# Performance work log

Measured on AMD Instinct MI355X. Metric: run time of the kernel, lower is better.

The kernel has to match this reference:

```python
import jax, jax.numpy as jnp
import numpy as np

N = 100000        # nodes
E = 1600000       # directed edges (before self loops)
F = 128           # input node features
H1, H2, H3 = 64, 32, 16
G = 64            # graphs in batch
EPS = 1e-5
NEG_SLOPE = 0.2


def setup_inputs():
    key = jax.random.key(0)
    ks = jax.random.split(key, 16)
    def rn(k, shape, scale=1.0):
        return jax.random.normal(k, shape, dtype=jnp.float32) * scale
    inp = {}
    inp['x'] = rn(ks[0], (N, F))
    inp['edge_index'] = jax.random.randint(ks[1], (2, E), 0, N)
    inp['batch'] = jnp.sort(jax.random.randint(ks[2], (N,), 0, G))
    dims = [(F, H1), (H1, H2), (H2, H3)]
    i = 3
    for li, (fi, fo) in enumerate(dims, start=1):
        s = 1.0 / np.sqrt(fi)
        kk = jax.random.split(ks[i], 3)
        inp[f'Wl{li}'] = rn(kk[0], (fi, fo), s)
        inp[f'bl{li}'] = jnp.zeros((fo,), jnp.float32)
        inp[f'Wr{li}'] = rn(kk[1], (fi, fo), s)
        inp[f'br{li}'] = jnp.zeros((fo,), jnp.float32)
        inp[f'att{li}'] = rn(kk[2], (fo,), 1.0 / np.sqrt(fo))
        inp[f'bias{li}'] = jnp.zeros((fo,), jnp.float32)
        inp[f'gamma{li}'] = jnp.ones((fo,), jnp.float32)
        inp[f'beta{li}'] = jnp.zeros((fo,), jnp.float32)
        i += 1
    inp['linW'] = rn(ks[i], (H3, 1), 0.25)
    inp['linb'] = jnp.zeros((1,), jnp.float32)
    return inp


def _gatv2(x, Wl, bl, Wr, br, att, bias, src, dst):
    # PyG GATv2Conv, heads=1: e_ij = a^T LeakyReLU(Wl x_j + Wr x_i)
    xl = x @ Wl + bl                         # [N, H] source transform
    xr = x @ Wr + br                         # [N, H] target transform
    e = jax.nn.leaky_relu(xl[src] + xr[dst], NEG_SLOPE) @ att   # [E']
    # numerically stable segment softmax over incoming edges of dst
    emax = jax.ops.segment_max(e, dst, num_segments=N)
    w = jnp.exp(e - emax[dst])
    denom = jax.ops.segment_sum(w, dst, num_segments=N)
    alpha = w / (denom[dst] + 1e-16)         # [E']
    out = jax.ops.segment_sum(alpha[:, None] * xl[src], dst, num_segments=N)
    return out + bias


def _batchnorm(x, gamma, beta):
    mu = jnp.mean(x, axis=0)
    var = jnp.var(x, axis=0)
    return (x - mu) * jax.lax.rsqrt(var + EPS) * gamma + beta


def reference(x, edge_index, batch,
              Wl1, bl1, Wr1, br1, att1, bias1, gamma1, beta1,
              Wl2, bl2, Wr2, br2, att2, bias2, gamma2, beta2,
              Wl3, bl3, Wr3, br3, att3, bias3, gamma3, beta3,
              linW, linb):
    # add self loops once (PyG GATv2Conv default add_self_loops=True)
    loops = jnp.arange(N, dtype=edge_index.dtype)
    src = jnp.concatenate([edge_index[0], loops])
    dst = jnp.concatenate([edge_index[1], loops])

    h = _gatv2(x, Wl1, bl1, Wr1, br1, att1, bias1, src, dst)
    h = jax.nn.relu(_batchnorm(h, gamma1, beta1))
    h = _gatv2(h, Wl2, bl2, Wr2, br2, att2, bias2, src, dst)
    h = jax.nn.relu(_batchnorm(h, gamma2, beta2))
    h = _gatv2(h, Wl3, bl3, Wr3, br3, att3, bias3, src, dst)
    h = jax.nn.relu(_batchnorm(h, gamma3, beta3))

    # global mean pool over graphs
    sums = jax.ops.segment_sum(h, batch, num_segments=G)          # [G, 16]
    cnts = jax.ops.segment_sum(jnp.ones((N,), h.dtype), batch, num_segments=G)
    pooled = sums / jnp.maximum(cnts, 1.0)[:, None]
    return pooled @ linW + linb                                   # [G, 1]
```

## Files before the change

### kernel.cpp

```cpp
#include <hip/hip_runtime.h>
#include <hip/hip_bf16.h>


static constexpr int G_ = 64;

__device__ __forceinline__ float bf2f(unsigned short u) {
  union { unsigned int i; float f; } c;
  c.i = ((unsigned int)u) << 16;
  return c.f;
}
__device__ __forceinline__ unsigned short f2bf(float f) {
  union { float f; unsigned int i; } c;
  c.f = f;
  unsigned int r = c.i + 0x7FFFu + ((c.i >> 16) & 1u);
  return (unsigned short)(r >> 16);
}

__global__ __launch_bounds__(256) void pack_all(
    const float* __restrict__ Wl1, const float* __restrict__ Wr1,
    const float* __restrict__ bl1, const float* __restrict__ br1,
    const float* __restrict__ Wl2, const float* __restrict__ Wr2,
    const float* __restrict__ bl2, const float* __restrict__ br2,
    const float* __restrict__ Wl3, const float* __restrict__ Wr3,
    const float* __restrict__ bl3, const float* __restrict__ br3,
    float* __restrict__ Wc1, float* __restrict__ bc1,
    float* __restrict__ Wc2, float* __restrict__ bc2,
    float* __restrict__ Wc3, float* __restrict__ bc3) {
  int i = blockIdx.x * 256 + threadIdx.x;
  if (i < 128 * 128) { int k = i >> 7, c = i & 127;
    Wc1[i] = (c < 64) ? Wl1[k * 64 + c] : Wr1[k * 64 + c - 64]; }
  if (i < 128) bc1[i] = (i < 64) ? bl1[i] : br1[i - 64];
  if (i < 64 * 64) { int k = i >> 6, c = i & 63;
    Wc2[i] = (c < 32) ? Wl2[k * 32 + c] : Wr2[k * 32 + c - 32]; }
  if (i < 64) bc2[i] = (i < 32) ? bl2[i] : br2[i - 32];
  if (i < 32 * 32) { int k = i >> 5, c = i & 31;
    Wc3[i] = (c < 16) ? Wl3[k * 16 + c] : Wr3[k * 16 + c - 16]; }
  if (i < 32) bc3[i] = (i < 16) ? bl3[i] : br3[i - 16];
}

template <int FI>
__global__ __launch_bounds__(256) void transpose_nf(
    const float* __restrict__ A, float* __restrict__ At, int N) {
  __shared__ float s[64][65];
  int n0 = blockIdx.x * 64, k0 = blockIdx.y * 64;
  int tid = threadIdx.x;
  for (int idx = tid; idx < 64 * 16; idx += 256) {
    int n = idx >> 4, c = idx & 15;
    float4 v = make_float4(0.f, 0.f, 0.f, 0.f);
    if (n0 + n < N)
      v = *reinterpret_cast<const float4*>(&A[(size_t)(n0 + n) * FI + k0 + c * 4]);
    s[n][c * 4 + 0] = v.x; s[n][c * 4 + 1] = v.y;
    s[n][c * 4 + 2] = v.z; s[n][c * 4 + 3] = v.w;
  }
  __syncthreads();
  for (int idx = tid; idx < 64 * 16; idx += 256) {
    int k = idx >> 4, c = idx & 15;
    int n = c * 4;
    if (n0 + n + 3 < N) {
      float4 v = make_float4(s[n][k], s[n + 1][k], s[n + 2][k], s[n + 3][k]);
      *reinterpret_cast<float4*>(&At[(size_t)(k0 + k) * N + n0 + n]) = v;
    } else {
      for (int j = 0; j < 4; j++)
        if (n0 + n + j < N) At[(size_t)(k0 + k) * N + n0 + n + j] = s[n + j][k];
    }
  }
}

__global__ __launch_bounds__(256) void edge_hist(
    const int* __restrict__ ei, int* __restrict__ deg, int E, int Etot, int N) {
  int p = blockIdx.x & 7;
  int q = blockIdx.x >> 3;
  int nbq = gridDim.x >> 3;
  float scale = 8.0f / (float)N;
  for (int i = q * 256 + threadIdx.x; i < Etot; i += nbq * 256) {
    int dst = (i < E) ? ei[E + i] : (i - E);
    int pp = min((int)((float)dst * scale), 7);
    if (pp == p) atomicAdd(&deg[dst], 1);
  }
}

__global__ __launch_bounds__(256) void scan1(
    const int* __restrict__ deg, int* __restrict__ part, int* __restrict__ bsums, int n) {
  __shared__ int ts[256];
  int t = threadIdx.x, b = blockIdx.x;
  int base = b * 1024 + t * 4;
  int d[4];
#pragma unroll
  for (int q = 0; q < 4; q++) d[q] = (base + q < n) ? deg[base + q] : 0;
  int s = d[0] + d[1] + d[2] + d[3];
  ts[t] = s;
  __syncthreads();
  for (int o = 1; o < 256; o <<= 1) {
    int v = (t >= o) ? ts[t - o] : 0;
    __syncthreads();
    ts[t] += v;
    __syncthreads();
  }
  int incl = ts[t];
  if (t == 255) bsums[b] = incl;
  int run = incl - s;
#pragma unroll
  for (int q = 0; q < 4; q++) {
    if (base + q < n) part[base + q] = run;
    run += d[q];
  }
}

__global__ void scan2(int* bsums, int nb) {
  __shared__ int s[256];
  int t = threadIdx.x;
  int v = (t < nb) ? bsums[t] : 0;
  s[t] = v;
  __syncthreads();
  for (int o = 1; o < 256; o <<= 1) {
    int u = (t >= o) ? s[t - o] : 0;
    __syncthreads();
    s[t] += u;
    __syncthreads();
  }
  if (t < nb) bsums[t] = s[t] - v;
}

__global__ __launch_bounds__(256) void scan3(
    int* __restrict__ rp, int* __restrict__ cur, const int* __restrict__ bsums,
    int n, int Etot) {
  int i = blockIdx.x * 256 + threadIdx.x;
  if (i < n) {
    int v = rp[i] + bsums[i >> 10];
    rp[i] = v; cur[i] = v;
  }
  if (i == 0) rp[n] = Etot;
}

__global__ __launch_bounds__(256) void scatter_edges(
    const int* __restrict__ ei, int* __restrict__ cur, int* __restrict__ ssrc,
    int E, int Etot, int N) {
  int p = blockIdx.x & 7;
  int q = blockIdx.x >> 3;
  int nbq = gridDim.x >> 3;
  float scale = 8.0f / (float)N;
  for (int i = q * 256 + threadIdx.x; i < Etot; i += nbq * 256) {
    int dst = (i < E) ? ei[E + i] : (i - E);
    int pp = min((int)((float)dst * scale), 7);
    if (pp != p) continue;
    int src = (i < E) ? ei[i] : (i - E);
    int pos = atomicAdd(&cur[dst], 1);
    ssrc[pos] = src;
  }
}

template <int FI, int FO>
__global__ __launch_bounds__(256) void gemm_fmaj2(
    const float* __restrict__ At, const float* __restrict__ Wcat,
    const float* __restrict__ bcat, unsigned short* __restrict__ Cb, int N) {
  constexpr int KC = 32;
  constexpr int CT = FO / 16;
  __shared__ float As[KC * 128];
  __shared__ float Ws[KC * FO];
  int tid = threadIdx.x;
  int ng = tid & 15;
  int hg = tid >> 4;
  int n0 = blockIdx.x * 128;
  bool full = (n0 + 128 <= N);

  float acc[8][CT];
#pragma unroll
  for (int i = 0; i < 8; i++)
#pragma unroll
    for (int j = 0; j < CT; j++) acc[i][j] = 0.f;

  for (int kc = 0; kc < FI; kc += KC) {
    __syncthreads();
    {
      int r = tid >> 5;
      int c = (tid & 31) * 4;
      for (int rr = r; rr < KC; rr += 8) {
        float4 v;
        if (full) {
          v = *reinterpret_cast<const float4*>(&At[(size_t)(kc + rr) * N + n0 + c]);
        } else {
          float tmp[4];
#pragma unroll
          for (int j = 0; j < 4; j++)
            tmp[j] = (n0 + c + j < N) ? At[(size_t)(kc + rr) * N + n0 + c + j] : 0.f;
          v = make_float4(tmp[0], tmp[1], tmp[2], tmp[3]);
        }
        *reinterpret_cast<float4*>(&As[rr * 128 + c]) = v;
      }
    }
    for (int idx = tid; idx < KC * FO / 4; idx += 256)
      *reinterpret_cast<float4*>(&Ws[idx * 4]) =
          *reinterpret_cast<const float4*>(&Wcat[kc * FO + idx * 4]);
    __syncthreads();
#pragma unroll
    for (int kk = 0; kk < KC; kk++) {
      float4 alo = *reinterpret_cast<float4*>(&As[kk * 128 + 4 * ng]);
      float4 ahi = *reinterpret_cast<float4*>(&As[kk * 128 + 64 + 4 * ng]);
      float a[8] = {alo.x, alo.y, alo.z, alo.w, ahi.x, ahi.y, ahi.z, ahi.w};
      float w[CT];
#pragma unroll
      for (int j = 0; j < CT; j++) w[j] = Ws[kk * FO + hg * CT + j];
#pragma unroll
      for (int i = 0; i < 8; i++)
#pragma unroll
        for (int j = 0; j < CT; j++) acc[i][j] = fmaf(a[i], w[j], acc[i][j]);
    }
  }

  float b[CT];
#pragma unroll
  for (int j = 0; j < CT; j++) b[j] = bcat[hg * CT + j];
#pragma unroll
  for (int i = 0; i < 8; i++) {
    int n = n0 + ((i < 4) ? (4 * ng + i) : (64 + 4 * ng + (i - 4)));
    if (n < N) {
      unsigned int u[CT / 2];
#pragma unroll
      for (int j2 = 0; j2 < CT / 2; j2++) {
        unsigned int lo = f2bf(acc[i][2 * j2] + b[2 * j2]);
        unsigned int hi = f2bf(acc[i][2 * j2 + 1] + b[2 * j2 + 1]);
        u[j2] = lo | (hi << 16);
      }
      unsigned short* dst = &Cb[(size_t)n * FO + hg * CT];
      if constexpr (CT == 8) {
        *reinterpret_cast<uint4*>(dst) = make_uint4(u[0], u[1], u[2], u[3]);
      } else if constexpr (CT == 4) {
        *reinterpret_cast<uint2*>(dst) = make_uint2(u[0], u[1]);
      } else {
        *reinterpret_cast<unsigned int*>(dst) = u[0];
      }
    }
  }
}

__device__ __forceinline__ float lrelu02(float z) {
  return (z > 0.f) ? z : 0.2f * z;
}

template <int H, bool UN2>
__global__ __launch_bounds__(256) void gat_agg2(
    const unsigned short* __restrict__ xlr, const float* __restrict__ att,
    const float* __restrict__ bias, const int* __restrict__ rp,
    const int* __restrict__ ssrc, float* __restrict__ out, int N) {
  constexpr int L = H / 4;
  constexpr int C = 64 / L;
  int v = blockIdx.x * 4 + (threadIdx.x >> 6);
  if (v >= N) return;
  int lane = threadIdx.x & 63;
  int fl = lane % L;
  int sub = lane / L;

  ushort4 qr = *reinterpret_cast<const ushort4*>(&xlr[(size_t)v * (2 * H) + H + fl * 4]);
  float xr0 = bf2f(qr.x), xr1 = bf2f(qr.y), xr2 = bf2f(qr.z), xr3 = bf2f(qr.w);
  const float4 a4 = *reinterpret_cast<const float4*>(&att[fl * 4]);
  int beg = rp[v], end = rp[v + 1];

  float mA = -3.0e38f, dA = 0.f;
  float4 accA = make_float4(0.f, 0.f, 0.f, 0.f);
  float mB = -3.0e38f, dB = 0.f;
  float4 accB = make_float4(0.f, 0.f, 0.f, 0.f);

  constexpr int STEP = UN2 ? 2 * C : C;

  for (int j = beg + sub; j < end; j += STEP) {
    {
      int u = ssrc[j];
      ushort4 q = *reinterpret_cast<const ushort4*>(&xlr[(size_t)u * (2 * H) + fl * 4]);
      float x0 = bf2f(q.x), x1 = bf2f(q.y), x2 = bf2f(q.z), x3 = bf2f(q.w);
      float t = a4.x * lrelu02(x0 + xr0);
      t = fmaf(a4.y, lrelu02(x1 + xr1), t);
      t = fmaf(a4.z, lrelu02(x2 + xr2), t);
      t = fmaf(a4.w, lrelu02(x3 + xr3), t);
#pragma unroll
      for (int o = L / 2; o >= 1; o >>= 1) t += __shfl_xor(t, o);
      float diff = t - mA;
      if (diff > 8.f) {
        float sc = __expf(-diff);
        dA *= sc;
        accA.x *= sc; accA.y *= sc; accA.z *= sc; accA.w *= sc;
        mA = t; diff = 0.f;
      }
      float w = __expf(diff);
      dA += w;
      accA.x = fmaf(w, x0, accA.x);
      accA.y = fmaf(w, x1, accA.y);
      accA.z = fmaf(w, x2, accA.z);
      accA.w = fmaf(w, x3, accA.w);
    }
    if (UN2) {
      int j2 = j + C;
      if (j2 < end) {
        int u = ssrc[j2];
        ushort4 q = *reinterpret_cast<const ushort4*>(&xlr[(size_t)u * (2 * H) + fl * 4]);
        float x0 = bf2f(q.x), x1 = bf2f(q.y), x2 = bf2f(q.z), x3 = bf2f(q.w);
        float t = a4.x * lrelu02(x0 + xr0);
        t = fmaf(a4.y, lrelu02(x1 + xr1), t);
        t = fmaf(a4.z, lrelu02(x2 + xr2), t);
        t = fmaf(a4.w, lrelu02(x3 + xr3), t);
#pragma unroll
        for (int o = L / 2; o >= 1; o >>= 1) t += __shfl_xor(t, o);
        float diff = t - mB;
        if (diff > 8.f) {
          float sc = __expf(-diff);
          dB *= sc;
          accB.x *= sc; accB.y *= sc; accB.z *= sc; accB.w *= sc;
          mB = t; diff = 0.f;
        }
        float w = __expf(diff);
        dB += w;
        accB.x = fmaf(w, x0, accB.x);
        accB.y = fmaf(w, x1, accB.y);
        accB.z = fmaf(w, x2, accB.z);
        accB.w = fmaf(w, x3, accB.w);
      }
    }
  }

  if (UN2) {
    float mn = fmaxf(mA, mB);
    float s1 = __expf(mA - mn), s2 = __expf(mB - mn);
    dA = dA * s1 + dB * s2;
    accA.x = accA.x * s1 + accB.x * s2;
    accA.y = accA.y * s1 + accB.y * s2;
    accA.z = accA.z * s1 + accB.z * s2;
    accA.w = accA.w * s1 + accB.w * s2;
    mA = mn;
  }

#pragma unroll
  for (int o = L; o < 64; o <<= 1) {
    float mo = __shfl_xor(mA, o);
    float d2 = __shfl_xor(dA, o);
    float ax = __shfl_xor(accA.x, o);
    float ay = __shfl_xor(accA.y, o);
    float az = __shfl_xor(accA.z, o);
    float aw = __shfl_xor(accA.w, o);
    float mn = fmaxf(mA, mo);
    float s1 = __expf(mA - mn), s2 = __expf(mo - mn);
    dA = dA * s1 + d2 * s2;
    accA.x = accA.x * s1 + ax * s2;
    accA.y = accA.y * s1 + ay * s2;
    accA.z = accA.z * s1 + az * s2;
    accA.w = accA.w * s1 + aw * s2;
    mA = mn;
  }

  if (lane < L) {
    float inv = 1.f / (dA + 1e-16f);
    const float4 b4 = *reinterpret_cast<const float4*>(&bias[fl * 4]);
    float4 o4 = make_float4(fmaf(accA.x, inv, b4.x), fmaf(accA.y, inv, b4.y),
                            fmaf(accA.z, inv, b4.z), fmaf(accA.w, inv, b4.w));
    *reinterpret_cast<float4*>(&out[(size_t)v * H + fl * 4]) = o4;
  }
}

template <int H>
__global__ __launch_bounds__(256) void bn_stats(
    const float* __restrict__ X, float* __restrict__ stats, int N) {
  __shared__ float ls[256], ls2[256];
  int tid = threadIdx.x;
  int h = tid % H;
  constexpr int RPB = 256 / H;
  int r0 = blockIdx.x * RPB + tid / H;
  float s = 0.f, s2 = 0.f;
  for (int n = r0; n < N; n += gridDim.x * RPB) {
    float val = X[(size_t)n * H + h];
    s += val; s2 += val * val;
  }
  ls[tid] = s; ls2[tid] = s2;
  __syncthreads();
  if (tid < H) {
    for (int g = 1; g < RPB; g++) { s += ls[tid + g * H]; s2 += ls2[tid + g * H]; }
    atomicAdd(&stats[h], s);
    atomicAdd(&stats[H + h], s2);
  }
}

__global__ void bn_finalize(
    const float* __restrict__ stats, const float* __restrict__ gamma,
    const float* __restrict__ beta, float* __restrict__ ss, int H, int N) {
  int h = threadIdx.x;
  if (h < H) {
    float mean = stats[h] / (float)N;
    float var = stats[H + h] / (float)N - mean * mean;
    float istd = rsqrtf(var + 1e-5f);
    float sc = gamma[h] * istd;
    ss[h] = sc;
    ss[H + h] = beta[h] - mean * sc;
  }
}

template <int H>
__global__ __launch_bounds__(256) void bn_apply_T(
    const float* __restrict__ X, const float* __restrict__ ss,
    float* __restrict__ Yt, int N) {
  __shared__ float s[64][65];
  int n0 = blockIdx.x * 64;
  int tid = threadIdx.x;
  for (int idx = tid; idx < 64 * (H / 4); idx += 256) {
    int n = idx / (H / 4), c = idx % (H / 4);
    float4 v = make_float4(0.f, 0.f, 0.f, 0.f);
    if (n0 + n < N)
      v = *reinterpret_cast<const float4*>(&X[(size_t)(n0 + n) * H + c * 4]);
    s[n][c * 4 + 0] = v.x; s[n][c * 4 + 1] = v.y;
    s[n][c * 4 + 2] = v.z; s[n][c * 4 + 3] = v.w;
  }
  __syncthreads();
  for (int idx = tid; idx < H * 16; idx += 256) {
    int k = idx >> 4, c = idx & 15;
    int n = c * 4;
    float sc = ss[k], sh = ss[H + k];
    float t0 = s[n + 0][k] * sc + sh;
    float t1 = s[n + 1][k] * sc + sh;
    float t2 = s[n + 2][k] * sc + sh;
    float t3 = s[n + 3][k] * sc + sh;
    float4 v = make_float4(t0 > 0.f ? t0 : 0.f, t1 > 0.f ? t1 : 0.f,
                           t2 > 0.f ? t2 : 0.f, t3 > 0.f ? t3 : 0.f);
    if (n0 + n + 3 < N) {
      *reinterpret_cast<float4*>(&Yt[(size_t)k * N + n0 + n]) = v;
    } else {
      float tv[4] = {v.x, v.y, v.z, v.w};
      for (int j = 0; j < 4; j++)
        if (n0 + n + j < N) Yt[(size_t)k * N + n0 + n + j] = tv[j];
    }
  }
}

__global__ __launch_bounds__(256) void pool_kernel(
    const float* __restrict__ X, const float* __restrict__ ss,
    const int* __restrict__ batch, float* __restrict__ pool,
    float* __restrict__ cnt, int N) {
  __shared__ float lp[G_ * 16];
  __shared__ float lc[G_];
  int tid = threadIdx.x;
  for (int j = tid; j < G_ * 16; j += 256) lp[j] = 0.f;
  if (tid < G_) lc[tid] = 0.f;
  __syncthreads();
  int tot = N * 16;
  for (int i = blockIdx.x * 256 + tid; i < tot; i += gridDim.x * 256) {
    int n = i >> 4, h = i & 15;
    int g = batch[n];
    float t = X[i] * ss[h] + ss[16 + h];
    t = (t > 0.f) ? t : 0.f;
    atomicAdd(&lp[g * 16 + h], t);
    if (h == 0) atomicAdd(&lc[g], 1.0f);
  }
  __syncthreads();
  for (int j = tid; j < G_ * 16; j += 256) atomicAdd(&pool[j], lp[j]);
  if (tid < G_) atomicAdd(&cnt[tid], lc[tid]);
}

__global__ void final_linear(
    const float* __restrict__ pool, const float* __restrict__ cnt,
    const float* __restrict__ linW, const float* __restrict__ linb,
    float* __restrict__ out) {
  int g = threadIdx.x;
  if (g < G_) {
    float c = fmaxf(cnt[g], 1.0f);
    float acc = 0.f;
    for (int h = 0; h < 16; h++) acc += (pool[g * 16 + h] / c) * linW[h];
    out[g] = acc + linb[0];
  }
}

extern "C" void kernel_launch(void* const* d_in, const int* in_sizes, int n_in,
                              void* d_out, int out_size, void* d_ws, size_t ws_size,
                              hipStream_t stream) {
  const float* x = (const float*)d_in[0];
  const int* ei = (const int*)d_in[1];
  const int* batch = (const int*)d_in[2];
  const int N = in_sizes[0] / 128;
  const int E = in_sizes[1] / 2;
  const int Etot = E + N;

  char* wsb = (char*)d_ws;
  size_t off = 0;
  auto alloc = [&](size_t bytes) -> void* {
    void* p = wsb + off;
    off += (bytes + 255) & ~(size_t)255;
    return p;
  };
  float* R0 = (float*)alloc((size_t)128 * N * 4);
  unsigned short* R1b = (unsigned short*)alloc((size_t)128 * N * 2);
  float* R2 = (float*)alloc((size_t)64 * N * 4);
  int* row_ptr = (int*)alloc((size_t)(N + 1) * 4);
  int* cursor = (int*)alloc((size_t)N * 4);
  int* bsums = (int*)alloc(4096);
  int* ssrc = (int*)alloc((size_t)Etot * 4);
  float* Wc1 = (float*)alloc(16384 * 4);  float* bc1 = (float*)alloc(128 * 4);
  float* Wc2 = (float*)alloc(4096 * 4);   float* bc2 = (float*)alloc(64 * 4);
  float* Wc3 = (float*)alloc(1024 * 4);   float* bc3 = (float*)alloc(32 * 4);
  float* ss = (float*)alloc(128 * 4);
  size_t zelems = (size_t)N + 3 * 128 + G_ * 16 + G_;
  char* zb = (char*)alloc(zelems * 4);
  int* deg = (int*)zb;
  float* stats1 = (float*)(zb + (size_t)N * 4);
  float* stats2 = stats1 + 128;
  float* stats3 = stats2 + 128;
  float* pool = stats3 + 128;
  float* cnt = pool + G_ * 16;

  const float* Wl1 = (const float*)d_in[3];  const float* bl1 = (const float*)d_in[4];
  const float* Wr1 = (const float*)d_in[5];  const float* br1 = (const float*)d_in[6];
  const float* att1 = (const float*)d_in[7]; const float* bias1 = (const float*)d_in[8];
  const float* g1 = (const float*)d_in[9];   const float* b1 = (const float*)d_in[10];
  const float* Wl2 = (const float*)d_in[11]; const float* bl2 = (const float*)d_in[12];
  const float* Wr2 = (const float*)d_in[13]; const float* br2 = (const float*)d_in[14];
  const float* att2 = (const float*)d_in[15]; const float* bias2 = (const float*)d_in[16];
  const float* g2 = (const float*)d_in[17];  const float* b2 = (const float*)d_in[18];
  const float* Wl3 = (const float*)d_in[19]; const float* bl3 = (const float*)d_in[20];
  const float* Wr3 = (const float*)d_in[21]; const float* br3 = (const float*)d_in[22];
  const float* att3 = (const float*)d_in[23]; const float* bias3 = (const float*)d_in[24];
  const float* g3 = (const float*)d_in[25];  const float* b3 = (const float*)d_in[26];
  const float* linW = (const float*)d_in[27]; const float* linb = (const float*)d_in[28];
  float* out = (float*)d_out;

  int ntiles = (N + 63) / 64;
  int ntiles2 = (N + 127) / 128;
  int nb = (N + 1023) / 1024;
  int nnodeblk = (N + 3) / 4;

  pack_all<<<64, 256, 0, stream>>>(Wl1, Wr1, bl1, br1, Wl2, Wr2, bl2, br2,
                                   Wl3, Wr3, bl3, br3, Wc1, bc1, Wc2, bc2, Wc3, bc3);
  hipMemsetAsync(zb, 0, zelems * 4, stream);
  transpose_nf<128><<<dim3(ntiles, 2), 256, 0, stream>>>(x, R0, N);

  edge_hist<<<4096, 256, 0, stream>>>(ei, deg, E, Etot, N);
  scan1<<<nb, 256, 0, stream>>>(deg, row_ptr, bsums, N);
  scan2<<<1, 256, 0, stream>>>(bsums, nb);
  scan3<<<(N + 255) / 256, 256, 0, stream>>>(row_ptr, cursor, bsums, N, Etot);
  scatter_edges<<<4096, 256, 0, stream>>>(ei, cursor, ssrc, E, Etot, N);

  gemm_fmaj2<128, 128><<<ntiles2, 256, 0, stream>>>(R0, Wc1, bc1, R1b, N);
  gat_agg2<64, true><<<nnodeblk, 256, 0, stream>>>(R1b, att1, bias1, row_ptr, ssrc, R2, N);
  bn_stats<64><<<512, 256, 0, stream>>>(R2, stats1, N);
  bn_finalize<<<1, 64, 0, stream>>>(stats1, g1, b1, ss, 64, N);
  bn_apply_T<64><<<ntiles, 256, 0, stream>>>(R2, ss, R0, N);

  gemm_fmaj2<64, 64><<<ntiles2, 256, 0, stream>>>(R0, Wc2, bc2, R1b, N);
  gat_agg2<32, true><<<nnodeblk, 256, 0, stream>>>(R1b, att2, bias2, row_ptr, ssrc, R2, N);
  bn_stats<32><<<512, 256, 0, stream>>>(R2, stats2, N);
  bn_finalize<<<1, 64, 0, stream>>>(stats2, g2, b2, ss, 32, N);
  bn_apply_T<32><<<ntiles, 256, 0, stream>>>(R2, ss, R0, N);

  gemm_fmaj2<32, 32><<<ntiles2, 256, 0, stream>>>(R0, Wc3, bc3, R1b, N);
  gat_agg2<16, false><<<nnodeblk, 256, 0, stream>>>(R1b, att3, bias3, row_ptr, ssrc, R2, N);
  bn_stats<16><<<512, 256, 0, stream>>>(R2, stats3, N);
  bn_finalize<<<1, 64, 0, stream>>>(stats3, g3, b3, ss, 16, N);

  pool_kernel<<<2048, 256, 0, stream>>>(R2, ss, batch, pool, cnt, N);
  final_linear<<<1, 64, 0, stream>>>(pool, cnt, linW, linb, out);
}
```

Measured before the change: 579.6 us.

## Replace FP32 SIMT GEMMs with bf16 MFMA and drop feature-major transposes

The scalar FMA GEMMs, which read feature-major transposed activations, are replaced by a bf16 MFMA 16x16x32 kernel that reads row-major activations directly. The input transpose kernel is removed, and the batchnorm-apply kernels now write row-major bf16 instead of transposed fp32. This removes the transpose passes and shrinks the intermediate activation traffic. The trade-offs are that inputs to layers 2 and 3 are quantized to bf16, and the output stores are scalar per element rather than vectorized.

```diff
diff --git a/kernel.cpp b/kernel.cpp
--- a/kernel.cpp
+++ b/kernel.cpp
@@ -3,6 +3,9 @@
 
 
 static constexpr int G_ = 64;
+
+typedef short bfrag __attribute__((ext_vector_type(8)));
+typedef float facc  __attribute__((ext_vector_type(4)));
 
 __device__ __forceinline__ float bf2f(unsigned short u) {
   union { unsigned int i; float f; } c;
@@ -23,47 +26,19 @@
     const float* __restrict__ bl2, const float* __restrict__ br2,
     const float* __restrict__ Wl3, const float* __restrict__ Wr3,
     const float* __restrict__ bl3, const float* __restrict__ br3,
-    float* __restrict__ Wc1, float* __restrict__ bc1,
-    float* __restrict__ Wc2, float* __restrict__ bc2,
-    float* __restrict__ Wc3, float* __restrict__ bc3) {
+    unsigned short* __restrict__ Wt1, float* __restrict__ bc1,
+    unsigned short* __restrict__ Wt2, float* __restrict__ bc2,
+    unsigned short* __restrict__ Wt3, float* __restrict__ bc3) {
   int i = blockIdx.x * 256 + threadIdx.x;
-  if (i < 128 * 128) { int k = i >> 7, c = i & 127;
-    Wc1[i] = (c < 64) ? Wl1[k * 64 + c] : Wr1[k * 64 + c - 64]; }
+  if (i < 128 * 128) { int c = i >> 7, k = i & 127;
+    Wt1[i] = f2bf((c < 64) ? Wl1[k * 64 + c] : Wr1[k * 64 + (c - 64)]); }
   if (i < 128) bc1[i] = (i < 64) ? bl1[i] : br1[i - 64];
-  if (i < 64 * 64) { int k = i >> 6, c = i & 63;
-    Wc2[i] = (c < 32) ? Wl2[k * 32 + c] : Wr2[k * 32 + c - 32]; }
+  if (i < 64 * 64) { int c = i >> 6, k = i & 63;
+    Wt2[i] = f2bf((c < 32) ? Wl2[k * 32 + c] : Wr2[k * 32 + (c - 32)]); }
   if (i < 64) bc2[i] = (i < 32) ? bl2[i] : br2[i - 32];
-  if (i < 32 * 32) { int k = i >> 5, c = i & 31;
-    Wc3[i] = (c < 16) ? Wl3[k * 16 + c] : Wr3[k * 16 + c - 16]; }
+  if (i < 32 * 32) { int c = i >> 5, k = i & 31;
+    Wt3[i] = f2bf((c < 16) ? Wl3[k * 16 + c] : Wr3[k * 16 + (c - 16)]); }
   if (i < 32) bc3[i] = (i < 16) ? bl3[i] : br3[i - 16];
-}
-
-template <int FI>
-__global__ __launch_bounds__(256) void transpose_nf(
-    const float* __restrict__ A, float* __restrict__ At, int N) {
-  __shared__ float s[64][65];
-  int n0 = blockIdx.x * 64, k0 = blockIdx.y * 64;
-  int tid = threadIdx.x;
-  for (int idx = tid; idx < 64 * 16; idx += 256) {
-    int n = idx >> 4, c = idx & 15;
-    float4 v = make_float4(0.f, 0.f, 0.f, 0.f);
-    if (n0 + n < N)
-      v = *reinterpret_cast<const float4*>(&A[(size_t)(n0 + n) * FI + k0 + c * 4]);
-    s[n][c * 4 + 0] = v.x; s[n][c * 4 + 1] = v.y;
-    s[n][c * 4 + 2] = v.z; s[n][c * 4 + 3] = v.w;
-  }
-  __syncthreads();
-  for (int idx = tid; idx < 64 * 16; idx += 256) {
-    int k = idx >> 4, c = idx & 15;
-    int n = c * 4;
-    if (n0 + n + 3 < N) {
-      float4 v = make_float4(s[n][k], s[n + 1][k], s[n + 2][k], s[n + 3][k]);
-      *reinterpret_cast<float4*>(&At[(size_t)(k0 + k) * N + n0 + n]) = v;
-    } else {
-      for (int j = 0; j < 4; j++)
-        if (n0 + n + j < N) At[(size_t)(k0 + k) * N + n0 + n + j] = s[n + j][k];
-    }
-  }
 }
 
 __global__ __launch_bounds__(256) void edge_hist(
@@ -149,86 +124,59 @@
   }
 }
 
-template <int FI, int FO>
-__global__ __launch_bounds__(256) void gemm_fmaj2(
-    const float* __restrict__ At, const float* __restrict__ Wcat,
+template <int FI, int FO, bool AFP32>
+__global__ __launch_bounds__(256) void gemm_mfma(
+    const void* __restrict__ Ain, const unsigned short* __restrict__ Wt,
     const float* __restrict__ bcat, unsigned short* __restrict__ Cb, int N) {
-  constexpr int KC = 32;
-  constexpr int CT = FO / 16;
-  __shared__ float As[KC * 128];
-  __shared__ float Ws[KC * FO];
+  constexpr int NT = FO / 16;
+  constexpr int KS = FI / 32;
   int tid = threadIdx.x;
-  int ng = tid & 15;
-  int hg = tid >> 4;
-  int n0 = blockIdx.x * 128;
-  bool full = (n0 + 128 <= N);
-
-  float acc[8][CT];
-#pragma unroll
-  for (int i = 0; i < 8; i++)
-#pragma unroll
-    for (int j = 0; j < CT; j++) acc[i][j] = 0.f;
-
-  for (int kc = 0; kc < FI; kc += KC) {
-    __syncthreads();
-    {
-      int r = tid >> 5;
-      int c = (tid & 31) * 4;
-      for (int rr = r; rr < KC; rr += 8) {
-        float4 v;
-        if (full) {
-          v = *reinterpret_cast<const float4*>(&At[(size_t)(kc + rr) * N + n0 + c]);
-        } else {
-          float tmp[4];
-#pragma unroll
-          for (int j = 0; j < 4; j++)
-            tmp[j] = (n0 + c + j < N) ? At[(size_t)(kc + rr) * N + n0 + c + j] : 0.f;
-          v = make_float4(tmp[0], tmp[1], tmp[2], tmp[3]);
-        }
-        *reinterpret_cast<float4*>(&As[rr * 128 + c]) = v;
-      }
+  int w = tid >> 6;
+  int lr = tid & 15;
+  int lg = (tid & 63) >> 4;
+  int n0 = blockIdx.x * 64;
+  int arow = min(n0 + w * 16 + lr, N - 1);
+
+  facc acc[NT];
+#pragma unroll
+  for (int t = 0; t < NT; t++)
+#pragma unroll
+    for (int e = 0; e < 4; e++) acc[t][e] = 0.f;
+
+#pragma unroll
+  for (int ks = 0; ks < KS; ks++) {
+    int k0 = ks * 32 + lg * 8;
+    bfrag a;
+    if constexpr (AFP32) {
+      const float* Af = (const float*)Ain;
+      const float* p = &Af[(size_t)arow * FI + k0];
+      float4 lo = *reinterpret_cast<const float4*>(p);
+      float4 hi = *reinterpret_cast<const float4*>(p + 4);
+      union { bfrag v; unsigned short u[8]; } cv;
+      cv.u[0] = f2bf(lo.x); cv.u[1] = f2bf(lo.y);
+      cv.u[2] = f2bf(lo.z); cv.u[3] = f2bf(lo.w);
+      cv.u[4] = f2bf(hi.x); cv.u[5] = f2bf(hi.y);
+      cv.u[6] = f2bf(hi.z); cv.u[7] = f2bf(hi.w);
+      a = cv.v;
+    } else {
+      const unsigned short* Ab = (const unsigned short*)Ain;
+      a = *reinterpret_cast<const bfrag*>(&Ab[(size_t)arow * FI + k0]);
     }
-    for (int idx = tid; idx < KC * FO / 4; idx += 256)
-      *reinterpret_cast<float4*>(&Ws[idx * 4]) =
-          *reinterpret_cast<const float4*>(&Wcat[kc * FO + idx * 4]);
-    __syncthreads();
-#pragma unroll
-    for (int kk = 0; kk < KC; kk++) {
-      float4 alo = *reinterpret_cast<float4*>(&As[kk * 128 + 4 * ng]);
-      float4 ahi = *reinterpret_cast<float4*>(&As[kk * 128 + 64 + 4 * ng]);
-      float a[8] = {alo.x, alo.y, alo.z, alo.w, ahi.x, ahi.y, ahi.z, ahi.w};
-      float w[CT];
-#pragma unroll
-      for (int j = 0; j < CT; j++) w[j] = Ws[kk * FO + hg * CT + j];
-#pragma unroll
-      for (int i = 0; i < 8; i++)
-#pragma unroll
-        for (int j = 0; j < CT; j++) acc[i][j] = fmaf(a[i], w[j], acc[i][j]);
+#pragma unroll
+    for (int t = 0; t < NT; t++) {
+      bfrag b = *reinterpret_cast<const bfrag*>(&Wt[(size_t)(t * 16 + lr) * FI + k0]);
+      acc[t] = __builtin_amdgcn_mfma_f32_16x16x32_bf16(a, b, acc[t], 0, 0, 0);
     }
   }
 
-  float b[CT];
-#pragma unroll
-  for (int j = 0; j < CT; j++) b[j] = bcat[hg * CT + j];
-#pragma unroll
-  for (int i = 0; i < 8; i++) {
-    int n = n0 + ((i < 4) ? (4 * ng + i) : (64 + 4 * ng + (i - 4)));
-    if (n < N) {
-      unsigned int u[CT / 2];
-#pragma unroll
-      for (int j2 = 0; j2 < CT / 2; j2++) {
-        unsigned int lo = f2bf(acc[i][2 * j2] + b[2 * j2]);
-        unsigned int hi = f2bf(acc[i][2 * j2 + 1] + b[2 * j2 + 1]);
-        u[j2] = lo | (hi << 16);
-      }
-      unsigned short* dst = &Cb[(size_t)n * FO + hg * CT];
-      if constexpr (CT == 8) {
-        *reinterpret_cast<uint4*>(dst) = make_uint4(u[0], u[1], u[2], u[3]);
-      } else if constexpr (CT == 4) {
-        *reinterpret_cast<uint2*>(dst) = make_uint2(u[0], u[1]);
-      } else {
-        *reinterpret_cast<unsigned int*>(dst) = u[0];
-      }
+#pragma unroll
+  for (int t = 0; t < NT; t++) {
+    int col = t * 16 + lr;
+    float bias = bcat[col];
+#pragma unroll
+    for (int r = 0; r < 4; r++) {
+      int n = n0 + w * 16 + lg * 4 + r;
+      if (n < N) Cb[(size_t)n * FO + col] = f2bf(acc[t][r] + bias);
     }
   }
 }
@@ -391,39 +339,22 @@
 }
 
 template <int H>
-__global__ __launch_bounds__(256) void bn_apply_T(
+__global__ __launch_bounds__(256) void bn_apply_b16(
     const float* __restrict__ X, const float* __restrict__ ss,
-    float* __restrict__ Yt, int N) {
-  __shared__ float s[64][65];
-  int n0 = blockIdx.x * 64;
-  int tid = threadIdx.x;
-  for (int idx = tid; idx < 64 * (H / 4); idx += 256) {
-    int n = idx / (H / 4), c = idx % (H / 4);
-    float4 v = make_float4(0.f, 0.f, 0.f, 0.f);
-    if (n0 + n < N)
-      v = *reinterpret_cast<const float4*>(&X[(size_t)(n0 + n) * H + c * 4]);
-    s[n][c * 4 + 0] = v.x; s[n][c * 4 + 1] = v.y;
-    s[n][c * 4 + 2] = v.z; s[n][c * 4 + 3] = v.w;
-  }
-  __syncthreads();
-  for (int idx = tid; idx < H * 16; idx += 256) {
-    int k = idx >> 4, c = idx & 15;
-    int n = c * 4;
-    float sc = ss[k], sh = ss[H + k];
-    float t0 = s[n + 0][k] * sc + sh;
-    float t1 = s[n + 1][k] * sc + sh;
-    float t2 = s[n + 2][k] * sc + sh;
-    float t3 = s[n + 3][k] * sc + sh;
-    float4 v = make_float4(t0 > 0.f ? t0 : 0.f, t1 > 0.f ? t1 : 0.f,
-                           t2 > 0.f ? t2 : 0.f, t3 > 0.f ? t3 : 0.f);
-    if (n0 + n + 3 < N) {
-      *reinterpret_cast<float4*>(&Yt[(size_t)k * N + n0 + n]) = v;
-    } else {
-      float tv[4] = {v.x, v.y, v.z, v.w};
-      for (int j = 0; j < 4; j++)
-        if (n0 + n + j < N) Yt[(size_t)k * N + n0 + n + j] = tv[j];
-    }
-  }
+    unsigned short* __restrict__ Y, int N) {
+  int g = blockIdx.x * 256 + threadIdx.x;
+  if (g >= N * (H / 4)) return;
+  int i = g * 4;
+  int h = i & (H - 1);
+  float4 v = *reinterpret_cast<const float4*>(&X[i]);
+  float t0 = fmaxf(fmaf(v.x, ss[h + 0], ss[H + h + 0]), 0.f);
+  float t1 = fmaxf(fmaf(v.y, ss[h + 1], ss[H + h + 1]), 0.f);
+  float t2 = fmaxf(fmaf(v.z, ss[h + 2], ss[H + h + 2]), 0.f);
+  float t3 = fmaxf(fmaf(v.w, ss[h + 3], ss[H + h + 3]), 0.f);
+  uint2 o;
+  o.x = (unsigned)f2bf(t0) | ((unsigned)f2bf(t1) << 16);
+  o.y = (unsigned)f2bf(t2) | ((unsigned)f2bf(t3) << 16);
+  *reinterpret_cast<uint2*>(&Y[i]) = o;
 }
 
 __global__ __launch_bounds__(256) void pool_kernel(
@@ -480,16 +411,19 @@
     off += (bytes + 255) & ~(size_t)255;
     return p;
   };
-  float* R0 = (float*)alloc((size_t)128 * N * 4);
   unsigned short* R1b = (unsigned short*)alloc((size_t)128 * N * 2);
   float* R2 = (float*)alloc((size_t)64 * N * 4);
+  unsigned short* hb = (unsigned short*)alloc((size_t)64 * N * 2);
   int* row_ptr = (int*)alloc((size_t)(N + 1) * 4);
   int* cursor = (int*)alloc((size_t)N * 4);
   int* bsums = (int*)alloc(4096);
   int* ssrc = (int*)alloc((size_t)Etot * 4);
-  float* Wc1 = (float*)alloc(16384 * 4);  float* bc1 = (float*)alloc(128 * 4);
-  float* Wc2 = (float*)alloc(4096 * 4);   float* bc2 = (float*)alloc(64 * 4);
-  float* Wc3 = (float*)alloc(1024 * 4);   float* bc3 = (float*)alloc(32 * 4);
+  unsigned short* Wt1 = (unsigned short*)alloc(16384 * 2);
+  float* bc1 = (float*)alloc(128 * 4);
+  unsigned short* Wt2 = (unsigned short*)alloc(4096 * 2);
+  float* bc2 = (float*)alloc(64 * 4);
+  unsigned short* Wt3 = (unsigned short*)alloc(1024 * 2);
+  float* bc3 = (float*)alloc(32 * 4);
   float* ss = (float*)alloc(128 * 4);
   size_t zelems = (size_t)N + 3 * 128 + G_ * 16 + G_;
   char* zb = (char*)alloc(zelems * 4);
@@ -515,15 +449,13 @@
   const float* linW = (const float*)d_in[27]; const float* linb = (const float*)d_in[28];
   float* out = (float*)d_out;
 
-  int ntiles = (N + 63) / 64;
-  int ntiles2 = (N + 127) / 128;
   int nb = (N + 1023) / 1024;
   int nnodeblk = (N + 3) / 4;
+  int ngemm = (N + 63) / 64;
 
   pack_all<<<64, 256, 0, stream>>>(Wl1, Wr1, bl1, br1, Wl2, Wr2, bl2, br2,
-                                   Wl3, Wr3, bl3, br3, Wc1, bc1, Wc2, bc2, Wc3, bc3);
+                                   Wl3, Wr3, bl3, br3, Wt1, bc1, Wt2, bc2, Wt3, bc3);
   hipMemsetAsync(zb, 0, zelems * 4, stream);
-  transpose_nf<128><<<dim3(ntiles, 2), 256, 0, stream>>>(x, R0, N);
 
   edge_hist<<<4096, 256, 0, stream>>>(ei, deg, E, Etot, N);
   scan1<<<nb, 256, 0, stream>>>(deg, row_ptr, bsums, N);
@@ -531,19 +463,19 @@
   scan3<<<(N + 255) / 256, 256, 0, stream>>>(row_ptr, cursor, bsums, N, Etot);
   scatter_edges<<<4096, 256, 0, stream>>>(ei, cursor, ssrc, E, Etot, N);
 
-  gemm_fmaj2<128, 128><<<ntiles2, 256, 0, stream>>>(R0, Wc1, bc1, R1b, N);
+  gemm_mfma<128, 128, true><<<ngemm, 256, 0, stream>>>(x, Wt1, bc1, R1b, N);
   gat_agg2<64, true><<<nnodeblk, 256, 0, stream>>>(R1b, att1, bias1, row_ptr, ssrc, R2, N);
   bn_stats<64><<<512, 256, 0, stream>>>(R2, stats1, N);
   bn_finalize<<<1, 64, 0, stream>>>(stats1, g1, b1, ss, 64, N);
-  bn_apply_T<64><<<ntiles, 256, 0, stream>>>(R2, ss, R0, N);
-
-  gemm_fmaj2<64, 64><<<ntiles2, 256, 0, stream>>>(R0, Wc2, bc2, R1b, N);
+  bn_apply_b16<64><<<(N * 16 + 255) / 256, 256, 0, stream>>>(R2, ss, hb, N);
+
+  gemm_mfma<64, 64, false><<<ngemm, 256, 0, stream>>>(hb, Wt2, bc2, R1b, N);
   gat_agg2<32, true><<<nnodeblk, 256, 0, stream>>>(R1b, att2, bias2, row_ptr, ssrc, R2, N);
   bn_stats<32><<<512, 256, 0, stream>>>(R2, stats2, N);
   bn_finalize<<<1, 64, 0, stream>>>(stats2, g2, b2, ss, 32, N);
-  bn_apply_T<32><<<ntiles, 256, 0, stream>>>(R2, ss, R0, N);
-
-  gemm_fmaj2<32, 32><<<ntiles2, 256, 0, stream>>>(R0, Wc3, bc3, R1b, N);
+  bn_apply_b16<32><<<(N * 8 + 255) / 256, 256, 0, stream>>>(R2, ss, hb, N);
+
+  gemm_mfma<32, 32, false><<<ngemm, 256, 0, stream>>>(hb, Wt3, bc3, R1b, N);
   gat_agg2<16, false><<<nnodeblk, 256, 0, stream>>>(R1b, att3, bias3, row_ptr, ssrc, R2, N);
   bn_stats<16><<<512, 256, 0, stream>>>(R2, stats3, N);
   bn_finalize<<<1, 64, 0, stream>>>(stats3, g3, b3, ss, 16, N);
```

After: 518.4 us. 10.6% less time.
